# Kernel optimization log

Hardware: AMD Instinct MI355X
Metric: run time of the kernel (lower is better)

## Reference

```python
import jax, jax.numpy as jnp
import numpy as np

B, L, D = 256, 512, 512

def setup_inputs() -> dict:
    key = jax.random.key(0)
    k1, k2, k3, k4, k5 = jax.random.split(key, 5)
    scale = 1.0 / np.sqrt(D)  # keep logits in a sane range
    return {
        "text_features": jax.random.normal(k1, (B, L, D), dtype=jnp.float32),
        "image_features": jax.random.normal(k2, (B, D), dtype=jnp.float32),
        "W_ML": jax.random.normal(k3, (D, D), dtype=jnp.float32) * scale,
        "W_MV": jax.random.normal(k4, (D, D), dtype=jnp.float32) * scale,
        "tau": jnp.ones((1,), dtype=jnp.float32),
        "padding_mask": jax.random.randint(k5, (B, L), 0, 2).astype(bool),
    }

def reference(text_features, image_features, W_ML, W_MV, tau, padding_mask):
    b, l, _ = text_features.shape
    tau_c = jnp.clip(tau, 0.001)  # [1]
    valid = ~padding_mask  # [B,L] True where token is real
    # Linear(bias=False): y = x @ W.T
    text_proj = jnp.einsum('bld,ed->ble', text_features, W_ML)   # [B,L,D]
    image_proj = jnp.einsum('bd,ed->be', image_features, W_MV)   # [B,D]
    neg_inf = jnp.float32(-jnp.inf)
    # positive scores: own image vs own text tokens
    s_iji = jnp.einsum('bd,bld->bl', image_proj, text_proj) / tau_c  # [B,L]
    # all-images-vs-text denominator: s_kji[i,l,k] = <text[i,l], image[k]>
    s_kji = jnp.einsum('ild,kd->ilk', text_proj, image_proj) / tau_c  # [B,L,B]
    mask_kj = valid.T[None, :, :]  # [1,L,B] -> valid[k,l] per (i,l,k)
    s_kji = jnp.where(mask_kj, s_kji, neg_inf)
    denom_log = jax.nn.logsumexp(s_kji, axis=2)  # [B,L]
    # cross-batch text negatives: s_iok[i,k,l] = <image[i], text[k,l]>
    s_iok = jnp.einsum('id,kld->ikl', image_proj, text_proj) / tau_c  # [B,B,L]
    mask_ko = valid[None, :, :]  # [1,B,L]
    mask_neq = ~jnp.eye(b, dtype=bool)[:, :, None]  # exclude k == i
    s_iok_f = jnp.where(mask_ko & mask_neq, s_iok, neg_inf).reshape(b, -1)
    cross_log = jax.nn.logsumexp(s_iok_f, axis=1)  # [B]
    neg_log = jnp.logaddexp(s_iji, cross_log[:, None])  # [B,L]
    denom_log = jnp.where(valid, denom_log, 0.0)
    neg_log = jnp.where(valid, neg_log, 0.0)
    f1 = denom_log - s_iji
    f2 = neg_log - s_iji
    loss_mat = 0.5 * (f1 + f2)
    n_valid = jnp.sum(valid)
    loss = jnp.sum(jnp.where(valid, loss_mat, 0.0)) / n_valid
    return loss
```

## Files before the change

### kernel.cpp

```cpp
#include <hip/hip_runtime.h>
#include <math.h>


#define B_ 256
#define L_ 512
#define D_ 512
#define ROWS (B_ * L_)
#define NT (ROWS / 64)
#define NEG_INF (-INFINITY)

typedef __attribute__((ext_vector_type(8))) short s8_t;
typedef __attribute__((ext_vector_type(4))) float f4_t;
typedef __attribute__((ext_vector_type(2))) float f2_t;
typedef __attribute__((ext_vector_type(4))) unsigned short us4_t;

__device__ inline unsigned short f2bf(float x) {
    unsigned int u = __float_as_uint(x);
    u += 0x7FFFu + ((u >> 16) & 1u);
    return (unsigned short)(u >> 16);
}

__global__ __launch_bounds__(256) void ip_kernel(const float* __restrict__ img,
                                                 const float* __restrict__ Wmv,
                                                 float* __restrict__ ip) {
    int kt = blockIdx.x >> 3, et = blockIdx.x & 7;
    __shared__ float Ast[32][36];
    __shared__ float Bst[32][72];
    int tid = threadIdx.x;
    int ty = tid >> 4;
    int tx = tid & 15;
    float acc[2][4] = {};
    int sr = tid >> 3, sc = (tid & 7) * 4;
    for (int d0 = 0; d0 < D_; d0 += 32) {
        f4_t a = *(const f4_t*)(img + (size_t)(kt * 32 + sr) * D_ + d0 + sc);
        f4_t b0 = *(const f4_t*)(Wmv + (size_t)(et * 64 + sr) * D_ + d0 + sc);
        f4_t b1 = *(const f4_t*)(Wmv + (size_t)(et * 64 + sr + 32) * D_ + d0 + sc);
        __syncthreads();
#pragma unroll
        for (int m = 0; m < 4; m++) {
            Ast[sc + m][sr] = a[m];
            Bst[sc + m][sr] = b0[m];
            Bst[sc + m][sr + 32] = b1[m];
        }
        __syncthreads();
#pragma unroll 4
        for (int d = 0; d < 32; d++) {
            f2_t a2 = *(const f2_t*)&Ast[d][ty * 2];
            f4_t b4 = *(const f4_t*)&Bst[d][tx * 4];
#pragma unroll
            for (int i = 0; i < 2; i++)
#pragma unroll
                for (int j = 0; j < 4; j++) acc[i][j] = fmaf(a2[i], b4[j], acc[i][j]);
        }
    }
#pragma unroll
    for (int i = 0; i < 2; i++) {
        f4_t o; o[0] = acc[i][0]; o[1] = acc[i][1]; o[2] = acc[i][2]; o[3] = acc[i][3];
        *(f4_t*)(ip + (size_t)(kt * 32 + ty * 2 + i) * D_ + et * 64 + tx * 4) = o;
    }
}

__global__ __launch_bounds__(256) void c_kernel(const float* __restrict__ ip,
                                                const float* __restrict__ Wml,
                                                const float* __restrict__ tau,
                                                unsigned short* __restrict__ Cb2) {
    int kt = blockIdx.x >> 3, dt = blockIdx.x & 7;
    __shared__ float Ast[32][36];
    __shared__ float Bst[32][72];
    int tid = threadIdx.x;
    int ty = tid >> 4;
    int tx = tid & 15;
    float acc[2][4] = {};
    int sr = tid >> 3, sc = (tid & 7) * 4;
    int br = tid >> 4, bc = (tid & 15) * 4;
    for (int e0 = 0; e0 < D_; e0 += 32) {
        f4_t a = *(const f4_t*)(ip + (size_t)(kt * 32 + sr) * D_ + e0 + sc);
        f4_t b0 = *(const f4_t*)(Wml + (size_t)(e0 + br) * D_ + dt * 64 + bc);
        f4_t b1 = *(const f4_t*)(Wml + (size_t)(e0 + br + 16) * D_ + dt * 64 + bc);
        __syncthreads();
#pragma unroll
        for (int m = 0; m < 4; m++) Ast[sc + m][sr] = a[m];
        *(f4_t*)&Bst[br][bc] = b0;
        *(f4_t*)&Bst[br + 16][bc] = b1;
        __syncthreads();
#pragma unroll 4
        for (int e = 0; e < 32; e++) {
            f2_t a2 = *(const f2_t*)&Ast[e][ty * 2];
            f4_t b4 = *(const f4_t*)&Bst[e][tx * 4];
#pragma unroll
            for (int i = 0; i < 2; i++)
#pragma unroll
                for (int j = 0; j < 4; j++) acc[i][j] = fmaf(a2[i], b4[j], acc[i][j]);
        }
    }
    float it = 1.0f / fmaxf(tau[0], 0.001f);
#pragma unroll
    for (int i = 0; i < 2; i++) {
        us4_t o;
#pragma unroll
        for (int j = 0; j < 4; j++) o[j] = f2bf(acc[i][j] * it);
        int n = kt * 32 + ty * 2 + i;
        int kk0 = dt * 64 + tx * 4;
        *(us4_t*)(Cb2 + (size_t)((kk0 >> 3) * 256 + n) * 8 + (kk0 & 7)) = o;
    }
}

__global__ __launch_bounds__(256) void mask_kernel(const int* __restrict__ pad,
                                                   unsigned long long* __restrict__ mbits) {
    int l = blockIdx.x;
    int w = threadIdx.x >> 6;
    int j = threadIdx.x & 63;
    unsigned long long bal = __ballot(pad[(w * 64 + j) * L_ + l] == 0);
    if (j == 0) mbits[l * 4 + w] = bal;
}

__global__ __launch_bounds__(128, 2) void gemm_mfma_kernel(
    const float* __restrict__ text, const unsigned short* __restrict__ Cb2,
    const unsigned long long* __restrict__ mbits,
    float* __restrict__ denom, float* __restrict__ siji,
    float* __restrict__ crossM, float* __restrict__ crossS) {
    __shared__ __align__(16) float lds[8512];
    float* Sh    = lds;
    float* pm    = lds + 8224;
    float* ps    = lds + 8352;
    float* rvadj = lds + 8480;

    const int tile = blockIdx.x;
    const int row0 = tile * 64;
    const int bIdx = row0 >> 9;
    const int l0 = row0 & 511;
    const int tid = threadIdx.x;
    const int wave = tid >> 6;
    const int lane = tid & 63;
    const int qd = lane >> 4;
    const int mm = lane & 15;

    f4_t acc[2][16];
#pragma unroll
    for (int mt = 0; mt < 2; mt++)
#pragma unroll
        for (int nt = 0; nt < 16; nt++)
#pragma unroll
            for (int r = 0; r < 4; r++) acc[mt][nt][r] = 0.f;

    const int wrow = row0 + wave * 32;
    const float* aB0 = text + (size_t)(wrow + mm) * D_ + qd * 8;
    const float* aB1 = aB0 + 16 * D_;
    const unsigned short* bB = Cb2 + qd * 2048 + mm * 8;

    f4_t ar[4];
    s8_t aa[2];
    s8_t bcur[8], bnxt[8];

#define LOAD_A(t) do { \
        ar[0] = *(const f4_t*)(aB0 + (t) * 32); \
        ar[1] = *(const f4_t*)(aB0 + (t) * 32 + 4); \
        ar[2] = *(const f4_t*)(aB1 + (t) * 32); \
        ar[3] = *(const f4_t*)(aB1 + (t) * 32 + 4); \
    } while (0)
#define LOAD_BH(dst, t, half) do { \
        _Pragma("unroll") \
        for (int nt = 0; nt < 8; nt++) \
            dst[nt] = *(const s8_t*)(bB + (t) * 8192 + (half) * 1024 + nt * 128); \
    } while (0)

    LOAD_A(0);
    LOAD_BH(bcur, 0, 0);
#pragma unroll 1
    for (int t = 0; t < 16; t++) {
        LOAD_BH(bnxt, t, 1);
#pragma unroll
        for (int q = 0; q < 2; q++) {
            s8_t a8;
#pragma unroll
            for (int j = 0; j < 4; j++) {
                a8[j]     = (short)f2bf(ar[2 * q][j]);
                a8[j + 4] = (short)f2bf(ar[2 * q + 1][j]);
            }
            aa[q] = a8;
        }
        int tn = (t + 1) & 15;
        LOAD_A(tn);
#pragma unroll
        for (int nt = 0; nt < 8; nt++) {
            acc[0][nt] = __builtin_amdgcn_mfma_f32_16x16x32_bf16(aa[0], bcur[nt], acc[0][nt], 0, 0, 0);
            acc[1][nt] = __builtin_amdgcn_mfma_f32_16x16x32_bf16(aa[1], bcur[nt], acc[1][nt], 0, 0, 0);
        }
        LOAD_BH(bcur, tn, 0);
#pragma unroll
        for (int nt = 0; nt < 8; nt++) {
            acc[0][8 + nt] = __builtin_amdgcn_mfma_f32_16x16x32_bf16(aa[0], bnxt[nt], acc[0][8 + nt], 0, 0, 0);
            acc[1][8 + nt] = __builtin_amdgcn_mfma_f32_16x16x32_bf16(aa[1], bnxt[nt], acc[1][8 + nt], 0, 0, 0);
        }
    }
#undef LOAD_A
#undef LOAD_BH

    float cm0 = NEG_INF, cs0 = 0.f, cm1 = NEG_INF, cs1 = 0.f;
    const int mw = bIdx >> 6, mb = bIdx & 63;

#pragma unroll
    for (int h = 0; h < 2; h++) {
        __syncthreads();
        if (wave == h) {
#pragma unroll
            for (int mt = 0; mt < 2; mt++)
#pragma unroll
                for (int nt = 0; nt < 16; nt++)
#pragma unroll
                    for (int r = 0; r < 4; r++)
                        Sh[(mt * 16 + qd * 4 + r) * 257 + nt * 16 + mm] = acc[mt][nt][r];
        }
        if (tid < 32) {
            int l = l0 + h * 32 + tid;
            rvadj[tid] = ((mbits[l * 4 + mw] >> mb) & 1ULL) ? 0.f : NEG_INF;
        }
        __syncthreads();

        {
            float m2 = NEG_INF, m3 = NEG_INF;
#pragma unroll 8
            for (int r = 0; r < 32; r++) {
                float adj = rvadj[r];
                m2 = fmaxf(m2, Sh[r * 257 + tid] + adj);
                m3 = fmaxf(m3, Sh[r * 257 + 128 + tid] + adj);
            }
            if (m2 > NEG_INF) {
                float s2 = 0.f;
#pragma unroll 8
                for (int r = 0; r < 32; r++)
                    s2 += __expf(Sh[r * 257 + tid] + rvadj[r] - m2);
                float M = fmaxf(cm0, m2);
                cs0 = cs0 * __expf(cm0 - M) + s2 * __expf(m2 - M);
                cm0 = M;
            }
            if (m3 > NEG_INF) {
                float s3 = 0.f;
#pragma unroll 8
                for (int r = 0; r < 32; r++)
                    s3 += __expf(Sh[r * 257 + 128 + tid] + rvadj[r] - m3);
                float M = fmaxf(cm1, m3);
                cs1 = cs1 * __expf(cm1 - M) + s3 * __expf(m3 - M);
                cm1 = M;
            }
        }
        {
            int row = tid & 31, grp = tid >> 5;
            int l = l0 + h * 32 + row;
            unsigned long long bits = mbits[l * 4 + grp];
            const float* Srow = Sh + row * 257 + grp * 64;
            float m = NEG_INF;
#pragma unroll 8
            for (int c = 0; c < 64; c++) {
                float adj = ((bits >> c) & 1ULL) ? 0.f : NEG_INF;
                m = fmaxf(m, Srow[c] + adj);
            }
            float s = 0.f;
            if (m > NEG_INF) {
#pragma unroll 8
                for (int c = 0; c < 64; c++) {
                    float adj = ((bits >> c) & 1ULL) ? 0.f : NEG_INF;
                    s += __expf(Srow[c] + adj - m);
                }
            }
            pm[grp * 32 + row] = m;
            ps[grp * 32 + row] = s;
        }
        __syncthreads();
        if (tid < 32) {
            float m0v = pm[tid], m1v = pm[32 + tid], m2v = pm[64 + tid], m3v = pm[96 + tid];
            float M = fmaxf(fmaxf(m0v, m1v), fmaxf(m2v, m3v));
            float dl;
            if (M == NEG_INF) dl = NEG_INF;
            else {
                float s = ps[tid] * __expf(m0v - M) + ps[32 + tid] * __expf(m1v - M) +
                          ps[64 + tid] * __expf(m2v - M) + ps[96 + tid] * __expf(m3v - M);
                dl = M + __logf(s);
            }
            int gr = row0 + h * 32 + tid;
            denom[gr] = dl;
            siji[gr] = Sh[tid * 257 + bIdx];
        }
    }
    if (tid == bIdx)       { cm0 = NEG_INF; cs0 = 0.f; }
    if (tid + 128 == bIdx) { cm1 = NEG_INF; cs1 = 0.f; }
    crossM[(size_t)tid * NT + tile] = cm0;
    crossS[(size_t)tid * NT + tile] = cs0;
    crossM[(size_t)(tid + 128) * NT + tile] = cm1;
    crossS[(size_t)(tid + 128) * NT + tile] = cs1;
}

__global__ __launch_bounds__(256) void cross_combine_kernel(const float* __restrict__ crossM,
                                                            const float* __restrict__ crossS,
                                                            float* __restrict__ crossLog) {
    int i = blockIdx.x;
    int tid = threadIdx.x;
    float m = NEG_INF, s = 0.f;
    for (int e = 0; e < NT / 256; e++) {
        int t = e * 256 + tid;
        float m2 = crossM[(size_t)i * NT + t];
        float s2 = crossS[(size_t)i * NT + t];
        if (m2 > NEG_INF) {
            if (m == NEG_INF) { m = m2; s = s2; }
            else {
                float M = fmaxf(m, m2);
                s = s * expf(m - M) + s2 * expf(m2 - M);
                m = M;
            }
        }
    }
    __shared__ float sm[256], ss[256];
    sm[tid] = m; ss[tid] = s;
    __syncthreads();
    for (int off = 128; off > 0; off >>= 1) {
        if (tid < off) {
            float m1 = sm[tid], s1 = ss[tid];
            float m2 = sm[tid + off], s2 = ss[tid + off];
            float M = fmaxf(m1, m2);
            float sv;
            if (M == NEG_INF) sv = 0.f;
            else sv = s1 * expf(m1 - M) + s2 * expf(m2 - M);
            sm[tid] = M; ss[tid] = sv;
        }
        __syncthreads();
    }
    if (tid == 0) crossLog[i] = (sm[0] == NEG_INF) ? NEG_INF : sm[0] + logf(ss[0]);
}

__global__ __launch_bounds__(256) void loss_partial_kernel(
    const int* __restrict__ pad, const float* __restrict__ denom,
    const float* __restrict__ siji, const float* __restrict__ crossLog,
    float* __restrict__ psum, float* __restrict__ pcnt) {
    int tid = threadIdx.x;
    int idx = blockIdx.x * 256 + tid;
    float term = 0.f, cnt = 0.f;
    if (pad[idx] == 0) {
        float dl = denom[idx], sv = siji[idx], cl = crossLog[idx >> 9];
        float M = fmaxf(sv, cl);
        float neg = M + log1pf(expf(-fabsf(sv - cl)));
        term = 0.5f * (dl + neg) - sv;
        cnt = 1.f;
    }
    __shared__ float bs[256], bc[256];
    bs[tid] = term; bc[tid] = cnt;
    __syncthreads();
    for (int off = 128; off > 0; off >>= 1) {
        if (tid < off) { bs[tid] += bs[tid + off]; bc[tid] += bc[tid + off]; }
        __syncthreads();
    }
    if (tid == 0) { psum[blockIdx.x] = bs[0]; pcnt[blockIdx.x] = bc[0]; }
}

__global__ __launch_bounds__(256) void final_kernel(const float* __restrict__ psum,
                                                    const float* __restrict__ pcnt,
                                                    float* __restrict__ out) {
    int tid = threadIdx.x;
    __shared__ float bs[256], bc[256];
    bs[tid] = psum[tid] + psum[tid + 256];
    bc[tid] = pcnt[tid] + pcnt[tid + 256];
    __syncthreads();
    for (int off = 128; off > 0; off >>= 1) {
        if (tid < off) { bs[tid] += bs[tid + off]; bc[tid] += bc[tid + off]; }
        __syncthreads();
    }
    if (tid == 0) out[0] = bs[0] / bc[0];
}

extern "C" void kernel_launch(void* const* d_in, const int* in_sizes, int n_in,
                              void* d_out, int out_size, void* d_ws, size_t ws_size,
                              hipStream_t stream) {
    (void)in_sizes; (void)n_in; (void)out_size; (void)ws_size;
    const float* text = (const float*)d_in[0];
    const float* img  = (const float*)d_in[1];
    const float* Wml  = (const float*)d_in[2];
    const float* Wmv  = (const float*)d_in[3];
    const float* tau  = (const float*)d_in[4];
    const int* pad    = (const int*)d_in[5];
    float* out = (float*)d_out;

    float* ws = (float*)d_ws;
    float* ip       = ws;
    unsigned short* Cb2 = (unsigned short*)(ws + 131072);
    unsigned long long* mbits = (unsigned long long*)(ws + 262144);
    float* denom    = ws + 266240;
    float* siji     = ws + 397312;
    float* crossM   = ws + 528384;
    float* crossS   = ws + 1052672;
    float* crossLog = ws + 1576960;
    float* psum     = ws + 1577216;
    float* pcnt     = ws + 1577728;

    hipLaunchKernelGGL(ip_kernel,   dim3(64),  dim3(256), 0, stream, img, Wmv, ip);
    hipLaunchKernelGGL(c_kernel,    dim3(64),  dim3(256), 0, stream, ip, Wml, tau, Cb2);
    hipLaunchKernelGGL(mask_kernel, dim3(L_),  dim3(256), 0, stream, pad, mbits);
    hipLaunchKernelGGL(gemm_mfma_kernel, dim3(NT), dim3(128), 0, stream,
                       text, Cb2, mbits, denom, siji, crossM, crossS);
    hipLaunchKernelGGL(cross_combine_kernel, dim3(B_), dim3(256), 0, stream,
                       crossM, crossS, crossLog);
    hipLaunchKernelGGL(loss_partial_kernel, dim3(ROWS / 256), dim3(256), 0, stream,
                       pad, denom, siji, crossLog, psum, pcnt);
    hipLaunchKernelGGL(final_kernel, dim3(1), dim3(256), 0, stream, psum, pcnt, out);
}
```

Measured before the change: 544.7 us.

## Stage B operand via LDS with direct global-to-LDS loads and register-level softmax reductions

The GEMM kernel now runs four waves per block in a 2x2 layout, so each wave covers 32 rows by 128 columns. The shared B operand is double-buffered into LDS with global_load_lds, replacing the per-wave global loads that made both waves in a block fetch the full B tile. The epilogue drops the 257-stride LDS score matrix and does the masked logsumexp reductions straight from accumulator registers with xor shuffles, merging per-wave partials through a small LDS area. The aims are to halve B global traffic per block, lower register pressure for better occupancy, and remove several LDS round trips and barriers, at the cost of a barrier on every K step.

```diff
diff --git a/kernel.cpp b/kernel.cpp
--- a/kernel.cpp
+++ b/kernel.cpp
@@ -13,6 +13,9 @@
 typedef __attribute__((ext_vector_type(4))) float f4_t;
 typedef __attribute__((ext_vector_type(2))) float f2_t;
 typedef __attribute__((ext_vector_type(4))) unsigned short us4_t;
+
+typedef __attribute__((address_space(3))) unsigned int lds_u32;
+typedef const __attribute__((address_space(1))) unsigned int glb_u32;
 
 __device__ inline unsigned short f2bf(float x) {
     unsigned int u = __float_as_uint(x);
@@ -114,16 +117,22 @@
     if (j == 0) mbits[l * 4 + w] = bal;
 }
 
-__global__ __launch_bounds__(128, 2) void gemm_mfma_kernel(
+#define ACC(mt, nt, r) ((mt) ? acc1[nt][r] : acc0[nt][r])
+
+#define MERGE_XOR(m, s, msk) do {                                        \
+        float mo_ = __shfl_xor(m, msk);                                  \
+        float so_ = __shfl_xor(s, msk);                                  \
+        float M_ = fmaxf(m, mo_);                                        \
+        s = (M_ > NEG_INF) ? (s * __expf(m - M_) + so_ * __expf(mo_ - M_)) : 0.f; \
+        m = M_;                                                          \
+    } while (0)
+
+__global__ __launch_bounds__(256, 3) void gemm_mfma_kernel(
     const float* __restrict__ text, const unsigned short* __restrict__ Cb2,
     const unsigned long long* __restrict__ mbits,
     float* __restrict__ denom, float* __restrict__ siji,
     float* __restrict__ crossM, float* __restrict__ crossS) {
-    __shared__ __align__(16) float lds[8512];
-    float* Sh    = lds;
-    float* pm    = lds + 8224;
-    float* ps    = lds + 8352;
-    float* rvadj = lds + 8480;
+    __shared__ __align__(16) unsigned char smem[32768];
 
     const int tile = blockIdx.x;
     const int row0 = tile * 64;
@@ -134,160 +143,162 @@
     const int lane = tid & 63;
     const int qd = lane >> 4;
     const int mm = lane & 15;
-
-    f4_t acc[2][16];
-#pragma unroll
-    for (int mt = 0; mt < 2; mt++)
-#pragma unroll
-        for (int nt = 0; nt < 16; nt++)
-#pragma unroll
-            for (int r = 0; r < 4; r++) acc[mt][nt][r] = 0.f;
-
-    const int wrow = row0 + wave * 32;
-    const float* aB0 = text + (size_t)(wrow + mm) * D_ + qd * 8;
-    const float* aB1 = aB0 + 16 * D_;
-    const unsigned short* bB = Cb2 + qd * 2048 + mm * 8;
+    const int wr = wave >> 1;
+    const int wc = wave & 1;
+
+    f4_t acc0[8], acc1[8];
+#pragma unroll
+    for (int nt = 0; nt < 8; nt++)
+#pragma unroll
+        for (int r = 0; r < 4; r++) { acc0[nt][r] = 0.f; acc1[nt][r] = 0.f; }
+
+    const float* aRow = text + (size_t)(row0 + wr * 32 + mm) * D_ + qd * 8;
 
     f4_t ar[4];
-    s8_t aa[2];
-    s8_t bcur[8], bnxt[8];
-
 #define LOAD_A(t) do { \
-        ar[0] = *(const f4_t*)(aB0 + (t) * 32); \
-        ar[1] = *(const f4_t*)(aB0 + (t) * 32 + 4); \
-        ar[2] = *(const f4_t*)(aB1 + (t) * 32); \
-        ar[3] = *(const f4_t*)(aB1 + (t) * 32 + 4); \
+        ar[0] = *(const f4_t*)(aRow + (t) * 32); \
+        ar[1] = *(const f4_t*)(aRow + (t) * 32 + 4); \
+        ar[2] = *(const f4_t*)(aRow + 16 * D_ + (t) * 32); \
+        ar[3] = *(const f4_t*)(aRow + 16 * D_ + (t) * 32 + 4); \
     } while (0)
-#define LOAD_BH(dst, t, half) do { \
+
+#define STAGE(buf, t) do { \
+        const unsigned char* gsrc_ = (const unsigned char*)Cb2 + (size_t)(t) * 16384 + wave * 1024 + lane * 16; \
+        unsigned char* ldst_ = smem + (buf) * 16384 + wave * 1024; \
         _Pragma("unroll") \
-        for (int nt = 0; nt < 8; nt++) \
-            dst[nt] = *(const s8_t*)(bB + (t) * 8192 + (half) * 1024 + nt * 128); \
+        for (int i_ = 0; i_ < 4; i_++) \
+            __builtin_amdgcn_global_load_lds((glb_u32*)(gsrc_ + i_ * 4096), \
+                                             (lds_u32*)(ldst_ + i_ * 4096), 16, 0, 0); \
     } while (0)
 
+    STAGE(0, 0);
     LOAD_A(0);
-    LOAD_BH(bcur, 0, 0);
+    int cur = 0;
 #pragma unroll 1
     for (int t = 0; t < 16; t++) {
-        LOAD_BH(bnxt, t, 1);
-#pragma unroll
-        for (int q = 0; q < 2; q++) {
-            s8_t a8;
-#pragma unroll
-            for (int j = 0; j < 4; j++) {
-                a8[j]     = (short)f2bf(ar[2 * q][j]);
-                a8[j + 4] = (short)f2bf(ar[2 * q + 1][j]);
+        __syncthreads();
+        if (t < 15) STAGE(cur ^ 1, t + 1);
+        s8_t aa0, aa1;
+#pragma unroll
+        for (int j = 0; j < 4; j++) {
+            aa0[j] = (short)f2bf(ar[0][j]); aa0[j + 4] = (short)f2bf(ar[1][j]);
+            aa1[j] = (short)f2bf(ar[2][j]); aa1[j + 4] = (short)f2bf(ar[3][j]);
+        }
+        if (t < 15) LOAD_A(t + 1);
+        const unsigned short* bbase =
+            (const unsigned short*)(smem + cur * 16384) + qd * 2048 + (wc * 128 + mm) * 8;
+#pragma unroll
+        for (int nt = 0; nt < 8; nt++) {
+            s8_t bf = *(const s8_t*)(bbase + nt * 128);
+            acc0[nt] = __builtin_amdgcn_mfma_f32_16x16x32_bf16(aa0, bf, acc0[nt], 0, 0, 0);
+            acc1[nt] = __builtin_amdgcn_mfma_f32_16x16x32_bf16(aa1, bf, acc1[nt], 0, 0, 0);
+        }
+        cur ^= 1;
+    }
+    __syncthreads();
+
+    float* fp  = (float*)smem;
+    float* pmp = fp;
+    float* psp = fp + 128;
+    float* cmp = fp + 256;
+    float* csp = fp + 768;
+
+    const int mw = bIdx >> 6, mb = bIdx & 63;
+
+    float radj[2][4];
+#pragma unroll
+    for (int mt = 0; mt < 2; mt++)
+#pragma unroll
+        for (int r = 0; r < 4; r++) {
+            int l = l0 + wr * 32 + mt * 16 + qd * 4 + r;
+            radj[mt][r] = ((mbits[l * 4 + mw] >> mb) & 1ULL) ? 0.f : NEG_INF;
+        }
+
+#pragma unroll
+    for (int nt = 0; nt < 8; nt++) {
+        float m = NEG_INF;
+#pragma unroll
+        for (int mt = 0; mt < 2; mt++)
+#pragma unroll
+            for (int r = 0; r < 4; r++) m = fmaxf(m, ACC(mt, nt, r) + radj[mt][r]);
+        float s = 0.f;
+        if (m > NEG_INF) {
+#pragma unroll
+            for (int mt = 0; mt < 2; mt++)
+#pragma unroll
+                for (int r = 0; r < 4; r++) s += __expf(ACC(mt, nt, r) + radj[mt][r] - m);
+        }
+        MERGE_XOR(m, s, 16);
+        MERGE_XOR(m, s, 32);
+        if (qd == 0) {
+            int col = wc * 128 + nt * 16 + mm;
+            cmp[wr * 256 + col] = m;
+            csp[wr * 256 + col] = s;
+        }
+    }
+
+#pragma unroll
+    for (int mt = 0; mt < 2; mt++)
+#pragma unroll
+        for (int r = 0; r < 4; r++) {
+            int rl = wr * 32 + mt * 16 + qd * 4 + r;
+            int l = l0 + rl;
+            unsigned long long w0 = mbits[l * 4 + wc * 2] >> mm;
+            unsigned long long w1 = mbits[l * 4 + wc * 2 + 1] >> mm;
+            float v[8];
+#pragma unroll
+            for (int nt = 0; nt < 4; nt++) {
+                v[nt]     = ACC(mt, nt, r)     + (((w0 >> (nt * 16)) & 1ULL) ? 0.f : NEG_INF);
+                v[nt + 4] = ((mt) ? acc1[nt + 4][r] : acc0[nt + 4][r])
+                            + (((w1 >> (nt * 16)) & 1ULL) ? 0.f : NEG_INF);
             }
-            aa[q] = a8;
-        }
-        int tn = (t + 1) & 15;
-        LOAD_A(tn);
-#pragma unroll
-        for (int nt = 0; nt < 8; nt++) {
-            acc[0][nt] = __builtin_amdgcn_mfma_f32_16x16x32_bf16(aa[0], bcur[nt], acc[0][nt], 0, 0, 0);
-            acc[1][nt] = __builtin_amdgcn_mfma_f32_16x16x32_bf16(aa[1], bcur[nt], acc[1][nt], 0, 0, 0);
-        }
-        LOAD_BH(bcur, tn, 0);
-#pragma unroll
-        for (int nt = 0; nt < 8; nt++) {
-            acc[0][8 + nt] = __builtin_amdgcn_mfma_f32_16x16x32_bf16(aa[0], bnxt[nt], acc[0][8 + nt], 0, 0, 0);
-            acc[1][8 + nt] = __builtin_amdgcn_mfma_f32_16x16x32_bf16(aa[1], bnxt[nt], acc[1][8 + nt], 0, 0, 0);
-        }
-    }
-#undef LOAD_A
-#undef LOAD_BH
-
-    float cm0 = NEG_INF, cs0 = 0.f, cm1 = NEG_INF, cs1 = 0.f;
-    const int mw = bIdx >> 6, mb = bIdx & 63;
-
-#pragma unroll
-    for (int h = 0; h < 2; h++) {
-        __syncthreads();
-        if (wave == h) {
-#pragma unroll
-            for (int mt = 0; mt < 2; mt++)
-#pragma unroll
-                for (int nt = 0; nt < 16; nt++)
-#pragma unroll
-                    for (int r = 0; r < 4; r++)
-                        Sh[(mt * 16 + qd * 4 + r) * 257 + nt * 16 + mm] = acc[mt][nt][r];
-        }
-        if (tid < 32) {
-            int l = l0 + h * 32 + tid;
-            rvadj[tid] = ((mbits[l * 4 + mw] >> mb) & 1ULL) ? 0.f : NEG_INF;
-        }
-        __syncthreads();
-
-        {
-            float m2 = NEG_INF, m3 = NEG_INF;
-#pragma unroll 8
-            for (int r = 0; r < 32; r++) {
-                float adj = rvadj[r];
-                m2 = fmaxf(m2, Sh[r * 257 + tid] + adj);
-                m3 = fmaxf(m3, Sh[r * 257 + 128 + tid] + adj);
-            }
-            if (m2 > NEG_INF) {
-                float s2 = 0.f;
-#pragma unroll 8
-                for (int r = 0; r < 32; r++)
-                    s2 += __expf(Sh[r * 257 + tid] + rvadj[r] - m2);
-                float M = fmaxf(cm0, m2);
-                cs0 = cs0 * __expf(cm0 - M) + s2 * __expf(m2 - M);
-                cm0 = M;
-            }
-            if (m3 > NEG_INF) {
-                float s3 = 0.f;
-#pragma unroll 8
-                for (int r = 0; r < 32; r++)
-                    s3 += __expf(Sh[r * 257 + 128 + tid] + rvadj[r] - m3);
-                float M = fmaxf(cm1, m3);
-                cs1 = cs1 * __expf(cm1 - M) + s3 * __expf(m3 - M);
-                cm1 = M;
-            }
-        }
-        {
-            int row = tid & 31, grp = tid >> 5;
-            int l = l0 + h * 32 + row;
-            unsigned long long bits = mbits[l * 4 + grp];
-            const float* Srow = Sh + row * 257 + grp * 64;
             float m = NEG_INF;
-#pragma unroll 8
-            for (int c = 0; c < 64; c++) {
-                float adj = ((bits >> c) & 1ULL) ? 0.f : NEG_INF;
-                m = fmaxf(m, Srow[c] + adj);
-            }
+#pragma unroll
+            for (int nt = 0; nt < 8; nt++) m = fmaxf(m, v[nt]);
             float s = 0.f;
             if (m > NEG_INF) {
-#pragma unroll 8
-                for (int c = 0; c < 64; c++) {
-                    float adj = ((bits >> c) & 1ULL) ? 0.f : NEG_INF;
-                    s += __expf(Srow[c] + adj - m);
-                }
+#pragma unroll
+                for (int nt = 0; nt < 8; nt++) s += __expf(v[nt] - m);
             }
-            pm[grp * 32 + row] = m;
-            ps[grp * 32 + row] = s;
-        }
-        __syncthreads();
-        if (tid < 32) {
-            float m0v = pm[tid], m1v = pm[32 + tid], m2v = pm[64 + tid], m3v = pm[96 + tid];
-            float M = fmaxf(fmaxf(m0v, m1v), fmaxf(m2v, m3v));
-            float dl;
-            if (M == NEG_INF) dl = NEG_INF;
-            else {
-                float s = ps[tid] * __expf(m0v - M) + ps[32 + tid] * __expf(m1v - M) +
-                          ps[64 + tid] * __expf(m2v - M) + ps[96 + tid] * __expf(m3v - M);
-                dl = M + __logf(s);
-            }
-            int gr = row0 + h * 32 + tid;
-            denom[gr] = dl;
-            siji[gr] = Sh[tid * 257 + bIdx];
-        }
-    }
-    if (tid == bIdx)       { cm0 = NEG_INF; cs0 = 0.f; }
-    if (tid + 128 == bIdx) { cm1 = NEG_INF; cs1 = 0.f; }
-    crossM[(size_t)tid * NT + tile] = cm0;
-    crossS[(size_t)tid * NT + tile] = cs0;
-    crossM[(size_t)(tid + 128) * NT + tile] = cm1;
-    crossS[(size_t)(tid + 128) * NT + tile] = cs1;
+            MERGE_XOR(m, s, 1);
+            MERGE_XOR(m, s, 2);
+            MERGE_XOR(m, s, 4);
+            MERGE_XOR(m, s, 8);
+            if (mm == 0) { pmp[wc * 64 + rl] = m; psp[wc * 64 + rl] = s; }
+        }
+
+#pragma unroll
+    for (int nt = 0; nt < 8; nt++)
+        if (wc == (bIdx >> 7) && mm == (bIdx & 15) && nt == ((bIdx >> 4) & 7)) {
+#pragma unroll
+            for (int mt = 0; mt < 2; mt++)
+#pragma unroll
+                for (int r = 0; r < 4; r++)
+                    siji[row0 + wr * 32 + mt * 16 + qd * 4 + r] = ACC(mt, nt, r);
+        }
+
+    __syncthreads();
+
+    if (tid < 64) {
+        float m0 = pmp[tid], m1 = pmp[64 + tid];
+        float s0 = psp[tid], s1 = psp[64 + tid];
+        float M = fmaxf(m0, m1);
+        float dl = NEG_INF;
+        if (M > NEG_INF) dl = M + __logf(s0 * __expf(m0 - M) + s1 * __expf(m1 - M));
+        denom[row0 + tid] = dl;
+    }
+    {
+        int col = tid;
+        float m0 = cmp[col], m1 = cmp[256 + col];
+        float s0 = csp[col], s1 = csp[256 + col];
+        float M = fmaxf(m0, m1);
+        float s = (M > NEG_INF) ? (s0 * __expf(m0 - M) + s1 * __expf(m1 - M)) : 0.f;
+        if (col == bIdx) { M = NEG_INF; s = 0.f; }
+        crossM[(size_t)col * NT + tile] = M;
+        crossS[(size_t)col * NT + tile] = s;
+    }
+#undef LOAD_A
+#undef STAGE
 }
 
 __global__ __launch_bounds__(256) void cross_combine_kernel(const float* __restrict__ crossM,
@@ -393,7 +404,7 @@
     hipLaunchKernelGGL(ip_kernel,   dim3(64),  dim3(256), 0, stream, img, Wmv, ip);
     hipLaunchKernelGGL(c_kernel,    dim3(64),  dim3(256), 0, stream, ip, Wml, tau, Cb2);
     hipLaunchKernelGGL(mask_kernel, dim3(L_),  dim3(256), 0, stream, pad, mbits);
-    hipLaunchKernelGGL(gemm_mfma_kernel, dim3(NT), dim3(128), 0, stream,
+    hipLaunchKernelGGL(gemm_mfma_kernel, dim3(NT), dim3(256), 0, stream,
                        text, Cb2, mbits, denom, siji, crossM, crossS);
     hipLaunchKernelGGL(cross_combine_kernel, dim3(B_), dim3(256), 0, stream,
                        crossM, crossS, crossLog);
```

Measured after the change: 462.2 us. 1.18x faster.
